# Performance work log

Hardware: AMD Instinct MI355X
Metric: run time of the kernel (lower is better)

## Reference

```python
import jax, jax.numpy as jnp
import numpy as np

IN_DIM = 512
ATT_DIM = 64
B, N = 4, 4096


def setup_inputs() -> dict:
    key = jax.random.key(0)
    k1, k2, k3, k4 = jax.random.split(key, 4)
    x = jax.random.normal(k1, (B, N, IN_DIM), dtype=jnp.float32)
    adj_matrix = (jax.random.uniform(k2, (B, N, N)) < 0.05).astype(jnp.float32)
    # nn.Linear weights: qk_nn (2*att_dim, in_dim), v_nn (in_dim, in_dim), no bias
    W_qk = jax.random.normal(k3, (2 * ATT_DIM, IN_DIM), dtype=jnp.float32) / np.sqrt(IN_DIM)
    W_v = jax.random.normal(k4, (IN_DIM, IN_DIM), dtype=jnp.float32) / np.sqrt(IN_DIM)
    return {"x": x, "adj_matrix": adj_matrix, "W_qk": W_qk, "W_v": W_v}


def reference(x, adj_matrix, W_qk, W_v):
    # q, k: (B, N, att_dim) from a single fused projection, then chunk
    qk = jnp.einsum('bnd,ed->bne', x, W_qk)
    q, k = jnp.split(qk, 2, axis=-1)
    v = jnp.einsum('bnd,ed->bne', x, W_v)  # (B, N, in_dim)
    inv_scale = 1.0 / (ATT_DIM ** 0.5)
    # dense NxN scores masked by adjacency, row-summed -> (B, N, 1)
    scores = jnp.einsum('bnd,bmd->bnm', q, k) * inv_scale
    w = jnp.sum(scores * adj_matrix, axis=-1, keepdims=True)
    w = jax.nn.softmax(w, axis=1)  # softmax over bag dimension N
    return w * v
```

## Files before the change

### kernel.cpp

```cpp
#include <hip/hip_runtime.h>
#include <hip/hip_bf16.h>

#define B_   4
#define N_   4096
#define IND  512
#define ATT  64
#define QKD  128

#define KSPLIT 4
#define KCHUNK 1024

typedef __attribute__((ext_vector_type(8))) short short8v;
typedef __attribute__((ext_vector_type(4))) float f32x4;

__device__ __forceinline__ void f8_to_bf16_hilo(const float4& v0, const float4& v1,
                                                short8v& hi, short8v& lo) {
  union { short8v v; unsigned short u[8]; } h, l;
  const float av[8] = {v0.x, v0.y, v0.z, v0.w, v1.x, v1.y, v1.z, v1.w};
#pragma unroll
  for (int j = 0; j < 8; ++j) {
    const unsigned short hu = (unsigned short)(__float_as_uint(av[j]) >> 16);
    const float fh = __uint_as_float((unsigned)hu << 16);
    h.u[j] = hu;
    l.u[j] = (unsigned short)(__float_as_uint(av[j] - fh) >> 16);
  }
  hi = h.v; lo = l.v;
}

__global__ __launch_bounds__(256)
void prep_frag(const float* __restrict__ src, unsigned short* __restrict__ dst,
               int nct) {
  const int wid = threadIdx.x >> 6, lane = threadIdx.x & 63;
  const int ct = blockIdx.x * 4 + wid;
  if (ct >= nct) return;
  const float* s = src + ((size_t)ct * 16 + (lane & 15)) * IND + ((lane >> 4) << 3);
  unsigned short* d = dst + (size_t)ct * 16 * 2 * 512 + (size_t)lane * 8;
#pragma unroll 4
  for (int slab = 0; slab < 16; ++slab) {
    const float4 v0 = *(const float4*)(s + slab * 32);
    const float4 v1 = *(const float4*)(s + slab * 32 + 4);
    short8v hv, lv;
    f8_to_bf16_hilo(v0, v1, hv, lv);
    *(short8v*)(d + (size_t)slab * 2 * 512)       = hv;
    *(short8v*)(d + (size_t)slab * 2 * 512 + 512) = lv;
  }
}

__global__ __launch_bounds__(256, 2)
void gemm_mfma(const unsigned short* __restrict__ xf,
               const unsigned short* __restrict__ wf,
               float* __restrict__ C, int Nout) {
  const int lane = threadIdx.x & 63;
  const int wid  = threadIdx.x >> 6;
  const int g0   = blockIdx.x * 64 + wid * 16;
  const int mt   = g0 >> 4;
  const int ct0  = blockIdx.y * 8;

  const unsigned short* xb = xf + (size_t)mt * 16 * 2 * 512 + (size_t)lane * 8;
  const unsigned short* wb = wf + (size_t)ct0 * 16 * 2 * 512 + (size_t)lane * 8;

  f32x4 acc[8] = {{0.f,0.f,0.f,0.f},{0.f,0.f,0.f,0.f},{0.f,0.f,0.f,0.f},
                  {0.f,0.f,0.f,0.f},{0.f,0.f,0.f,0.f},{0.f,0.f,0.f,0.f},
                  {0.f,0.f,0.f,0.f},{0.f,0.f,0.f,0.f}};

  short8v axh = *(const short8v*)(xb);
  short8v axl = *(const short8v*)(xb + 512);

  for (int slab = 0; slab < 16; ++slab) {
    const int sn = (slab < 15) ? slab + 1 : 15;
    const short8v nxh = *(const short8v*)(xb + (size_t)sn * 1024);
    const short8v nxl = *(const short8v*)(xb + (size_t)sn * 1024 + 512);

#pragma unroll
    for (int c = 0; c < 8; ++c) {
      const unsigned short* wp = wb + ((size_t)(c * 16 + slab) * 2) * 512;
      const short8v bh = *(const short8v*)(wp);
      const short8v bl = *(const short8v*)(wp + 512);
      acc[c] = __builtin_amdgcn_mfma_f32_16x16x32_bf16(axh, bh, acc[c], 0, 0, 0);
      acc[c] = __builtin_amdgcn_mfma_f32_16x16x32_bf16(axl, bh, acc[c], 0, 0, 0);
      acc[c] = __builtin_amdgcn_mfma_f32_16x16x32_bf16(axh, bl, acc[c], 0, 0, 0);
    }
    axh = nxh; axl = nxl;
  }

  float* outp = C + ((size_t)g0 + ((lane >> 4) << 2)) * Nout + ct0 * 16 + (lane & 15);
#pragma unroll
  for (int c = 0; c < 8; ++c)
#pragma unroll
    for (int r = 0; r < 4; ++r)
      outp[(size_t)r * Nout + c * 16] = acc[c][r];
}

__global__ __launch_bounds__(256)
void prep_k(const float* __restrict__ qk, unsigned short* __restrict__ ktf) {
  __shared__ unsigned short sh[32][68];
  __shared__ unsigned short sl[32][68];
  const int b    = blockIdx.x >> 7;
  const int slab = blockIdx.x & 127;
  const int t = threadIdx.x;

#pragma unroll
  for (int i = 0; i < 2; ++i) {
    const int f = t + i * 256;
    const int ml  = f >> 4;
    const int ch4 = (f & 15) << 2;
    const float4 v = *(const float4*)(qk +
        ((size_t)b * N_ + slab * 32 + ml) * QKD + ATT + ch4);
    const float vv[4] = {v.x, v.y, v.z, v.w};
#pragma unroll
    for (int j = 0; j < 4; ++j) {
      const unsigned short hi = (unsigned short)(__float_as_uint(vv[j]) >> 16);
      const float fhi = __uint_as_float((unsigned)hi << 16);
      const unsigned short lo = (unsigned short)(__float_as_uint(vv[j] - fhi) >> 16);
      sh[ml][ch4 + j] = hi;
      sl[ml][ch4 + j] = lo;
    }
  }
  __syncthreads();

  const int lane = t & 63;
  const int c    = t >> 6;
  const int mb   = (lane >> 4) << 3;
  const int ch   = c * 16 + (lane & 15);
  unsigned short* outb = ktf +
      (((size_t)(b * 128 + slab) * 4 + c) * 2) * 512 + (size_t)lane * 8;
  union { short8v v; unsigned short u[8]; } hv, lv;
#pragma unroll
  for (int j = 0; j < 8; ++j) {
    hv.u[j] = sh[mb + j][ch];
    lv.u[j] = sl[mb + j][ch];
  }
  *(short8v*)(outb)       = hv.v;
  *(short8v*)(outb + 512) = lv.v;
}

__global__ __launch_bounds__(256, 2)
void adjk_mfma(const float* __restrict__ adj,
               const unsigned short* __restrict__ ktf,
               float* __restrict__ kapart) {
  const int lane = threadIdx.x & 63;
  const int wid  = threadIdx.x >> 6;
  const int g0   = blockIdx.x * 128 + wid * 32;
  const int b    = g0 >> 12;
  const int split = blockIdx.y;
  const int k0   = split * KCHUNK;
  const int slab0 = k0 >> 5;

  const int arow = lane & 15;
  const int koff = (lane >> 4) << 3;

  const float* aptr0 = adj + (size_t)(g0 + arow) * N_ + k0 + koff;
  const float* aptr1 = aptr0 + (size_t)16 * N_;
  const unsigned short* kbase =
      ktf + (size_t)(b * 128 + slab0) * 4096 + (size_t)lane * 8;

  f32x4 acc[2][4] = {{{0.f,0.f,0.f,0.f},{0.f,0.f,0.f,0.f},
                      {0.f,0.f,0.f,0.f},{0.f,0.f,0.f,0.f}},
                     {{0.f,0.f,0.f,0.f},{0.f,0.f,0.f,0.f},
                      {0.f,0.f,0.f,0.f},{0.f,0.f,0.f,0.f}}};

  float4 a00 = *(const float4*)(aptr0);
  float4 a01 = *(const float4*)(aptr0 + 4);
  float4 a10 = *(const float4*)(aptr1);
  float4 a11 = *(const float4*)(aptr1 + 4);

  for (int s = 0; s < 32; ++s) {
    const unsigned short* kb = kbase + (size_t)s * 4096;
    const short8v b00 = *(const short8v*)(kb);
    const short8v b01 = *(const short8v*)(kb + 512);
    const short8v b10 = *(const short8v*)(kb + 1024);
    const short8v b11 = *(const short8v*)(kb + 1536);
    const short8v b20 = *(const short8v*)(kb + 2048);
    const short8v b21 = *(const short8v*)(kb + 2560);
    const short8v b30 = *(const short8v*)(kb + 3072);
    const short8v b31 = *(const short8v*)(kb + 3584);

    const int sn = (s < 31) ? s + 1 : 31;
    const float4 n00 = *(const float4*)(aptr0 + sn * 32);
    const float4 n01 = *(const float4*)(aptr0 + sn * 32 + 4);
    const float4 n10 = *(const float4*)(aptr1 + sn * 32);
    const float4 n11 = *(const float4*)(aptr1 + sn * 32 + 4);

    union { short8v v; unsigned short u[8]; } af0, af1;
    {
      const float av0[8] = {a00.x,a00.y,a00.z,a00.w,a01.x,a01.y,a01.z,a01.w};
      const float av1[8] = {a10.x,a10.y,a10.z,a10.w,a11.x,a11.y,a11.z,a11.w};
#pragma unroll
      for (int j = 0; j < 8; ++j) {
        af0.u[j] = (unsigned short)(__float_as_uint(av0[j]) >> 16);
        af1.u[j] = (unsigned short)(__float_as_uint(av1[j]) >> 16);
      }
    }

    acc[0][0] = __builtin_amdgcn_mfma_f32_16x16x32_bf16(af0.v, b00, acc[0][0], 0,0,0);
    acc[0][0] = __builtin_amdgcn_mfma_f32_16x16x32_bf16(af0.v, b01, acc[0][0], 0,0,0);
    acc[0][1] = __builtin_amdgcn_mfma_f32_16x16x32_bf16(af0.v, b10, acc[0][1], 0,0,0);
    acc[0][1] = __builtin_amdgcn_mfma_f32_16x16x32_bf16(af0.v, b11, acc[0][1], 0,0,0);
    acc[0][2] = __builtin_amdgcn_mfma_f32_16x16x32_bf16(af0.v, b20, acc[0][2], 0,0,0);
    acc[0][2] = __builtin_amdgcn_mfma_f32_16x16x32_bf16(af0.v, b21, acc[0][2], 0,0,0);
    acc[0][3] = __builtin_amdgcn_mfma_f32_16x16x32_bf16(af0.v, b30, acc[0][3], 0,0,0);
    acc[0][3] = __builtin_amdgcn_mfma_f32_16x16x32_bf16(af0.v, b31, acc[0][3], 0,0,0);
    acc[1][0] = __builtin_amdgcn_mfma_f32_16x16x32_bf16(af1.v, b00, acc[1][0], 0,0,0);
    acc[1][0] = __builtin_amdgcn_mfma_f32_16x16x32_bf16(af1.v, b01, acc[1][0], 0,0,0);
    acc[1][1] = __builtin_amdgcn_mfma_f32_16x16x32_bf16(af1.v, b10, acc[1][1], 0,0,0);
    acc[1][1] = __builtin_amdgcn_mfma_f32_16x16x32_bf16(af1.v, b11, acc[1][1], 0,0,0);
    acc[1][2] = __builtin_amdgcn_mfma_f32_16x16x32_bf16(af1.v, b20, acc[1][2], 0,0,0);
    acc[1][2] = __builtin_amdgcn_mfma_f32_16x16x32_bf16(af1.v, b21, acc[1][2], 0,0,0);
    acc[1][3] = __builtin_amdgcn_mfma_f32_16x16x32_bf16(af1.v, b30, acc[1][3], 0,0,0);
    acc[1][3] = __builtin_amdgcn_mfma_f32_16x16x32_bf16(af1.v, b31, acc[1][3], 0,0,0);

    a00 = n00; a01 = n01; a10 = n10; a11 = n11;
  }

#pragma unroll
  for (int tile = 0; tile < 2; ++tile) {
    float* outp = kapart +
        ((size_t)split * (B_ * N_) + g0 + tile * 16 + ((lane >> 4) << 2)) * ATT
        + (lane & 15);
#pragma unroll
    for (int c = 0; c < 4; ++c)
#pragma unroll
      for (int r = 0; r < 4; ++r)
        outp[(size_t)r * ATT + c * 16] = acc[tile][c][r];
  }
}

__global__ __launch_bounds__(256)
void qdot(const float* __restrict__ qk, const float* __restrict__ kapart,
          float* __restrict__ wpre) {
  const int wid  = threadIdx.x >> 6;
  const int lane = threadIdx.x & 63;
  const int row  = blockIdx.x * 4 + wid;

  float ka = 0.f;
#pragma unroll
  for (int s = 0; s < KSPLIT; ++s)
    ka += kapart[((size_t)s * B_ * N_ + row) * ATT + lane];

  const float q = qk[(size_t)row * QKD + lane];
  float val = q * ka;
#pragma unroll
  for (int off = 32; off; off >>= 1) val += __shfl_xor(val, off);
  if (lane == 0) wpre[row] = val * 0.125f;
}

__global__ __launch_bounds__(256)
void softmax_bag(float* __restrict__ w) {
  __shared__ float red[256];
  const int b = blockIdx.x;
  float* wb = w + (size_t)b * N_;
  const int t = threadIdx.x;

  float vals[16];
  float mx = -1e30f;
#pragma unroll
  for (int i = 0; i < 16; ++i) {
    vals[i] = wb[t + i * 256];
    mx = fmaxf(mx, vals[i]);
  }
  red[t] = mx; __syncthreads();
  for (int s = 128; s; s >>= 1) {
    if (t < s) red[t] = fmaxf(red[t], red[t + s]);
    __syncthreads();
  }
  mx = red[0];
  __syncthreads();

  float sum = 0.f;
#pragma unroll
  for (int i = 0; i < 16; ++i) {
    vals[i] = expf(vals[i] - mx);
    sum += vals[i];
  }
  red[t] = sum; __syncthreads();
  for (int s = 128; s; s >>= 1) {
    if (t < s) red[t] += red[t + s];
    __syncthreads();
  }
  const float inv = 1.f / red[0];
#pragma unroll
  for (int i = 0; i < 16; ++i) wb[t + i * 256] = vals[i] * inv;
}

__global__ __launch_bounds__(256)
void scale_v(float* __restrict__ out, const float* __restrict__ w, int total4) {
  int idx = blockIdx.x * blockDim.x + threadIdx.x;
  const int stride = gridDim.x * blockDim.x;
  for (; idx < total4; idx += stride) {
    float4 v = ((const float4*)out)[idx];
    const float s = w[idx >> 7];
    v.x *= s; v.y *= s; v.z *= s; v.w *= s;
    ((float4*)out)[idx] = v;
  }
}

extern "C" void kernel_launch(void* const* d_in, const int* in_sizes, int n_in,
                              void* d_out, int out_size, void* d_ws, size_t ws_size,
                              hipStream_t stream) {
  const float* x    = (const float*)d_in[0];
  const float* adj  = (const float*)d_in[1];
  const float* W_qk = (const float*)d_in[2];
  const float* W_v  = (const float*)d_in[3];
  float* out = (float*)d_out;

  float* qk     = (float*)d_ws;
  float* kapart = qk + (size_t)B_ * N_ * QKD;
  float* wpre   = kapart + (size_t)KSPLIT * B_ * N_ * ATT;
  unsigned short* ktf  = (unsigned short*)(wpre + B_ * N_);
  unsigned short* xft  = ktf + (size_t)B_ * 128 * 4096;
  unsigned short* wvf  = xft + (size_t)1024 * 16 * 2 * 512;
  unsigned short* wqkf = wvf + (size_t)32 * 16 * 2 * 512;

  const int M = B_ * N_;

  prep_frag<<<256, 256, 0, stream>>>(x, xft, 1024);
  prep_frag<<<8, 256, 0, stream>>>(W_v, wvf, 32);
  prep_frag<<<2, 256, 0, stream>>>(W_qk, wqkf, 8);

  {
    dim3 grid(M / 64, QKD / 128);
    gemm_mfma<<<grid, 256, 0, stream>>>(xft, wqkf, qk, QKD);
  }
  {
    dim3 grid(M / 64, IND / 128);
    gemm_mfma<<<grid, 256, 0, stream>>>(xft, wvf, out, IND);
  }
  prep_k<<<B_ * 128, 256, 0, stream>>>(qk, ktf);
  {
    dim3 grid(M / 128, KSPLIT);
    adjk_mfma<<<grid, 256, 0, stream>>>(adj, ktf, kapart);
  }
  qdot<<<M / 4, 256, 0, stream>>>(qk, kapart, wpre);
  softmax_bag<<<B_, 256, 0, stream>>>(wpre);
  const int total4 = M * (IND / 4);
  scale_v<<<2048, 256, 0, stream>>>(out, wpre, total4);
}
```

Measured before the change: 518.9 us.

## Stage adj/K tiles via async global-to-LDS loads and fuse softmax scaling into V GEMM

Replaces the register-prefetch adj×K kernel with an LDS double-buffered version that uses global_load_lds with an XOR swizzle to bring adjacency and K fragments into shared memory. KSPLIT drops from 4 to 2, so each block walks a longer K range and there are fewer partial sums. The V projection GEMM now runs after the softmax and multiplies by the weights in its epilogue, which removes the separate scale_v read-modify-write pass over the output. The 96KB shared-memory footprint limits occupancy to one block per CU and halves the grid of the dominant kernel.

```diff
diff --git a/kernel.cpp b/kernel.cpp
--- a/kernel.cpp
+++ b/kernel.cpp
@@ -7,11 +7,18 @@
 #define ATT  64
 #define QKD  128
 
-#define KSPLIT 4
-#define KCHUNK 1024
+#define KSPLIT 2
+#define KCHUNK 2048
+#define AK_NT  32
 
 typedef __attribute__((ext_vector_type(8))) short short8v;
 typedef __attribute__((ext_vector_type(4))) float f32x4;
+
+__device__ __forceinline__ void gload_lds16(const void* g, void* l) {
+  __builtin_amdgcn_global_load_lds(
+      (const __attribute__((address_space(1))) unsigned int*)g,
+      (__attribute__((address_space(3))) unsigned int*)l, 16, 0, 0);
+}
 
 __device__ __forceinline__ void f8_to_bf16_hilo(const float4& v0, const float4& v1,
                                                 short8v& hi, short8v& lo) {
@@ -49,7 +56,8 @@
 __global__ __launch_bounds__(256, 2)
 void gemm_mfma(const unsigned short* __restrict__ xf,
                const unsigned short* __restrict__ wf,
-               float* __restrict__ C, int Nout) {
+               float* __restrict__ C, int Nout,
+               const float* __restrict__ wsc) {
   const int lane = threadIdx.x & 63;
   const int wid  = threadIdx.x >> 6;
   const int g0   = blockIdx.x * 64 + wid * 16;
@@ -85,10 +93,12 @@
 
   float* outp = C + ((size_t)g0 + ((lane >> 4) << 2)) * Nout + ct0 * 16 + (lane & 15);
 #pragma unroll
-  for (int c = 0; c < 8; ++c)
-#pragma unroll
-    for (int r = 0; r < 4; ++r)
-      outp[(size_t)r * Nout + c * 16] = acc[c][r];
+  for (int r = 0; r < 4; ++r) {
+    const float s = wsc ? wsc[g0 + ((lane >> 4) << 2) + r] : 1.0f;
+#pragma unroll
+    for (int c = 0; c < 8; ++c)
+      outp[(size_t)r * Nout + c * 16] = acc[c][r] * s;
+  }
 }
 
 __global__ __launch_bounds__(256)
@@ -134,94 +144,106 @@
   *(short8v*)(outb + 512) = lv.v;
 }
 
-__global__ __launch_bounds__(256, 2)
-void adjk_mfma(const float* __restrict__ adj,
-               const unsigned short* __restrict__ ktf,
-               float* __restrict__ kapart) {
+__global__ __launch_bounds__(256)
+void adjk_lds(const float* __restrict__ adj,
+              const unsigned short* __restrict__ ktf,
+              float* __restrict__ kapart) {
+  __shared__ __align__(16) unsigned char smem[98304];
   const int lane = threadIdx.x & 63;
   const int wid  = threadIdx.x >> 6;
-  const int g0   = blockIdx.x * 128 + wid * 32;
+  const int g0   = blockIdx.x * 128;
   const int b    = g0 >> 12;
   const int split = blockIdx.y;
   const int k0   = split * KCHUNK;
-  const int slab0 = k0 >> 5;
-
-  const int arow = lane & 15;
-  const int koff = (lane >> 4) << 3;
-
-  const float* aptr0 = adj + (size_t)(g0 + arow) * N_ + k0 + koff;
-  const float* aptr1 = aptr0 + (size_t)16 * N_;
-  const unsigned short* kbase =
-      ktf + (size_t)(b * 128 + slab0) * 4096 + (size_t)lane * 8;
+
+  const int lr   = lane >> 4;
+  const int cch  = lane & 15;
+
+  auto STAGE = [&](int t, int buf) {
+    const int kt = k0 + t * 64;
+    {
+      const int rbase = wid * 32;
+#pragma unroll
+      for (int i = 0; i < 8; ++i) {
+        const int r = rbase + i * 4 + lr;
+        const int csrc = cch ^ (r & 7);
+        const float* src = adj + (size_t)(g0 + r) * N_ + kt + csrc * 4;
+        void* dst = smem + buf * 32768 + (rbase + i * 4) * 256;
+        gload_lds16(src, dst);
+      }
+    }
+    {
+      const unsigned short* kb = ktf + ((size_t)b * 128 + (kt >> 5)) * 4096;
+#pragma unroll
+      for (int j = 0; j < 4; ++j) {
+        const unsigned short* src = kb + (wid * 4 + j) * 512 + lane * 8;
+        void* dst = smem + 65536 + buf * 16384 + (wid * 4 + j) * 1024;
+        gload_lds16(src, dst);
+      }
+    }
+  };
 
   f32x4 acc[2][4] = {{{0.f,0.f,0.f,0.f},{0.f,0.f,0.f,0.f},
                       {0.f,0.f,0.f,0.f},{0.f,0.f,0.f,0.f}},
                      {{0.f,0.f,0.f,0.f},{0.f,0.f,0.f,0.f},
                       {0.f,0.f,0.f,0.f},{0.f,0.f,0.f,0.f}}};
 
-  float4 a00 = *(const float4*)(aptr0);
-  float4 a01 = *(const float4*)(aptr0 + 4);
-  float4 a10 = *(const float4*)(aptr1);
-  float4 a11 = *(const float4*)(aptr1 + 4);
-
-  for (int s = 0; s < 32; ++s) {
-    const unsigned short* kb = kbase + (size_t)s * 4096;
-    const short8v b00 = *(const short8v*)(kb);
-    const short8v b01 = *(const short8v*)(kb + 512);
-    const short8v b10 = *(const short8v*)(kb + 1024);
-    const short8v b11 = *(const short8v*)(kb + 1536);
-    const short8v b20 = *(const short8v*)(kb + 2048);
-    const short8v b21 = *(const short8v*)(kb + 2560);
-    const short8v b30 = *(const short8v*)(kb + 3072);
-    const short8v b31 = *(const short8v*)(kb + 3584);
-
-    const int sn = (s < 31) ? s + 1 : 31;
-    const float4 n00 = *(const float4*)(aptr0 + sn * 32);
-    const float4 n01 = *(const float4*)(aptr0 + sn * 32 + 4);
-    const float4 n10 = *(const float4*)(aptr1 + sn * 32);
-    const float4 n11 = *(const float4*)(aptr1 + sn * 32 + 4);
-
-    union { short8v v; unsigned short u[8]; } af0, af1;
-    {
-      const float av0[8] = {a00.x,a00.y,a00.z,a00.w,a01.x,a01.y,a01.z,a01.w};
-      const float av1[8] = {a10.x,a10.y,a10.z,a10.w,a11.x,a11.y,a11.z,a11.w};
-#pragma unroll
-      for (int j = 0; j < 8; ++j) {
-        af0.u[j] = (unsigned short)(__float_as_uint(av0[j]) >> 16);
-        af1.u[j] = (unsigned short)(__float_as_uint(av1[j]) >> 16);
+  STAGE(0, 0);
+  __syncthreads();
+
+  for (int t = 0; t < AK_NT; ++t) {
+    const int cur = t & 1;
+    if (t + 1 < AK_NT) STAGE(t + 1, cur ^ 1);
+
+    const float* A = (const float*)(smem + cur * 32768);
+    const unsigned short* Bp = (const unsigned short*)(smem + 65536 + cur * 16384);
+
+#pragma unroll
+    for (int s2 = 0; s2 < 2; ++s2) {
+      const unsigned short* bb = Bp + s2 * 4096 + lane * 8;
+      const short8v b0h = *(const short8v*)(bb);
+      const short8v b0l = *(const short8v*)(bb + 512);
+      const short8v b1h = *(const short8v*)(bb + 1024);
+      const short8v b1l = *(const short8v*)(bb + 1536);
+      const short8v b2h = *(const short8v*)(bb + 2048);
+      const short8v b2l = *(const short8v*)(bb + 2560);
+      const short8v b3h = *(const short8v*)(bb + 3072);
+      const short8v b3l = *(const short8v*)(bb + 3584);
+
+#pragma unroll
+      for (int rt = 0; rt < 2; ++rt) {
+        const int r = wid * 32 + rt * 16 + cch;
+        const int cb = s2 * 8 + (lr << 1);
+        const f32x4 a0 = *(const f32x4*)(A + r * 64 + ((cb ^ (r & 7)) << 2));
+        const f32x4 a1 = *(const f32x4*)(A + r * 64 + (((cb + 1) ^ (r & 7)) << 2));
+        union { short8v v; unsigned short u[8]; } af;
+#pragma unroll
+        for (int j = 0; j < 4; ++j) {
+          af.u[j]     = (unsigned short)(__float_as_uint(a0[j]) >> 16);
+          af.u[4 + j] = (unsigned short)(__float_as_uint(a1[j]) >> 16);
+        }
+        acc[rt][0] = __builtin_amdgcn_mfma_f32_16x16x32_bf16(af.v, b0h, acc[rt][0], 0,0,0);
+        acc[rt][0] = __builtin_amdgcn_mfma_f32_16x16x32_bf16(af.v, b0l, acc[rt][0], 0,0,0);
+        acc[rt][1] = __builtin_amdgcn_mfma_f32_16x16x32_bf16(af.v, b1h, acc[rt][1], 0,0,0);
+        acc[rt][1] = __builtin_amdgcn_mfma_f32_16x16x32_bf16(af.v, b1l, acc[rt][1], 0,0,0);
+        acc[rt][2] = __builtin_amdgcn_mfma_f32_16x16x32_bf16(af.v, b2h, acc[rt][2], 0,0,0);
+        acc[rt][2] = __builtin_amdgcn_mfma_f32_16x16x32_bf16(af.v, b2l, acc[rt][2], 0,0,0);
+        acc[rt][3] = __builtin_amdgcn_mfma_f32_16x16x32_bf16(af.v, b3h, acc[rt][3], 0,0,0);
+        acc[rt][3] = __builtin_amdgcn_mfma_f32_16x16x32_bf16(af.v, b3l, acc[rt][3], 0,0,0);
       }
     }
-
-    acc[0][0] = __builtin_amdgcn_mfma_f32_16x16x32_bf16(af0.v, b00, acc[0][0], 0,0,0);
-    acc[0][0] = __builtin_amdgcn_mfma_f32_16x16x32_bf16(af0.v, b01, acc[0][0], 0,0,0);
-    acc[0][1] = __builtin_amdgcn_mfma_f32_16x16x32_bf16(af0.v, b10, acc[0][1], 0,0,0);
-    acc[0][1] = __builtin_amdgcn_mfma_f32_16x16x32_bf16(af0.v, b11, acc[0][1], 0,0,0);
-    acc[0][2] = __builtin_amdgcn_mfma_f32_16x16x32_bf16(af0.v, b20, acc[0][2], 0,0,0);
-    acc[0][2] = __builtin_amdgcn_mfma_f32_16x16x32_bf16(af0.v, b21, acc[0][2], 0,0,0);
-    acc[0][3] = __builtin_amdgcn_mfma_f32_16x16x32_bf16(af0.v, b30, acc[0][3], 0,0,0);
-    acc[0][3] = __builtin_amdgcn_mfma_f32_16x16x32_bf16(af0.v, b31, acc[0][3], 0,0,0);
-    acc[1][0] = __builtin_amdgcn_mfma_f32_16x16x32_bf16(af1.v, b00, acc[1][0], 0,0,0);
-    acc[1][0] = __builtin_amdgcn_mfma_f32_16x16x32_bf16(af1.v, b01, acc[1][0], 0,0,0);
-    acc[1][1] = __builtin_amdgcn_mfma_f32_16x16x32_bf16(af1.v, b10, acc[1][1], 0,0,0);
-    acc[1][1] = __builtin_amdgcn_mfma_f32_16x16x32_bf16(af1.v, b11, acc[1][1], 0,0,0);
-    acc[1][2] = __builtin_amdgcn_mfma_f32_16x16x32_bf16(af1.v, b20, acc[1][2], 0,0,0);
-    acc[1][2] = __builtin_amdgcn_mfma_f32_16x16x32_bf16(af1.v, b21, acc[1][2], 0,0,0);
-    acc[1][3] = __builtin_amdgcn_mfma_f32_16x16x32_bf16(af1.v, b30, acc[1][3], 0,0,0);
-    acc[1][3] = __builtin_amdgcn_mfma_f32_16x16x32_bf16(af1.v, b31, acc[1][3], 0,0,0);
-
-    a00 = n00; a01 = n01; a10 = n10; a11 = n11;
-  }
-
-#pragma unroll
-  for (int tile = 0; tile < 2; ++tile) {
+    __syncthreads();
+  }
+
+#pragma unroll
+  for (int rt = 0; rt < 2; ++rt) {
     float* outp = kapart +
-        ((size_t)split * (B_ * N_) + g0 + tile * 16 + ((lane >> 4) << 2)) * ATT
-        + (lane & 15);
+        ((size_t)split * (B_ * N_) + g0 + wid * 32 + rt * 16 + (lr << 2)) * ATT + cch;
 #pragma unroll
     for (int c = 0; c < 4; ++c)
 #pragma unroll
       for (int r = 0; r < 4; ++r)
-        outp[(size_t)r * ATT + c * 16] = acc[tile][c][r];
+        outp[(size_t)r * ATT + c * 16] = acc[rt][c][r];
   }
 }
 
@@ -280,18 +302,6 @@
   const float inv = 1.f / red[0];
 #pragma unroll
   for (int i = 0; i < 16; ++i) wb[t + i * 256] = vals[i] * inv;
-}
-
-__global__ __launch_bounds__(256)
-void scale_v(float* __restrict__ out, const float* __restrict__ w, int total4) {
-  int idx = blockIdx.x * blockDim.x + threadIdx.x;
-  const int stride = gridDim.x * blockDim.x;
-  for (; idx < total4; idx += stride) {
-    float4 v = ((const float4*)out)[idx];
-    const float s = w[idx >> 7];
-    v.x *= s; v.y *= s; v.z *= s; v.w *= s;
-    ((float4*)out)[idx] = v;
-  }
 }
 
 extern "C" void kernel_launch(void* const* d_in, const int* in_sizes, int n_in,
@@ -319,19 +329,17 @@
 
   {
     dim3 grid(M / 64, QKD / 128);
-    gemm_mfma<<<grid, 256, 0, stream>>>(xft, wqkf, qk, QKD);
-  }
-  {
-    dim3 grid(M / 64, IND / 128);
-    gemm_mfma<<<grid, 256, 0, stream>>>(xft, wvf, out, IND);
+    gemm_mfma<<<grid, 256, 0, stream>>>(xft, wqkf, qk, QKD, nullptr);
   }
   prep_k<<<B_ * 128, 256, 0, stream>>>(qk, ktf);
   {
     dim3 grid(M / 128, KSPLIT);
-    adjk_mfma<<<grid, 256, 0, stream>>>(adj, ktf, kapart);
+    adjk_lds<<<grid, 256, 0, stream>>>(adj, ktf, kapart);
   }
   qdot<<<M / 4, 256, 0, stream>>>(qk, kapart, wpre);
   softmax_bag<<<B_, 256, 0, stream>>>(wpre);
-  const int total4 = M * (IND / 4);
-  scale_v<<<2048, 256, 0, stream>>>(out, wpre, total4);
-}
+  {
+    dim3 grid(M / 64, IND / 128);
+    gemm_mfma<<<grid, 256, 0, stream>>>(xft, wvf, out, IND, wpre);
+  }
+}
```

New measurement: 514.6 us. Within noise of the previous version (-0.8%).

## Bit-pack adjacency into a mask and fuse softmax scaling into the V GEMM

Applied to the files above, without the earlier changes.

Adds a streaming pass that compresses the fp32 adjacency into one bit per entry. The adj·K MFMA kernel then reads that 8 MB mask and expands the bits into bf16 ones and zeros, instead of loading and truncating fp32 tiles inside the MFMA loop. It also reorders the launches so the softmax weights exist before the V projection, which applies them as a per-row scale in its epilogue and removes the separate scale_v pass over the output. The mask only holds for binary adjacency values, and the full fp32 adjacency is still read once by the new packing kernel.

```diff
diff --git a/kernel.cpp b/kernel.cpp
--- a/kernel.cpp
+++ b/kernel.cpp
@@ -25,6 +25,27 @@
     l.u[j] = (unsigned short)(__float_as_uint(av[j] - fh) >> 16);
   }
   hi = h.v; lo = l.v;
+}
+
+__global__ __launch_bounds__(256)
+void pack_adj(const float* __restrict__ adj, unsigned char* __restrict__ mask) {
+  const size_t total = (size_t)B_ * N_ * (N_ / 8);
+  size_t i = (size_t)blockIdx.x * 256 + threadIdx.x;
+  const size_t stride = (size_t)gridDim.x * 256;
+  for (; i < total; i += stride) {
+    const float4 v0 = *(const float4*)(adj + i * 8);
+    const float4 v1 = *(const float4*)(adj + i * 8 + 4);
+    unsigned b = 0;
+    b |= (v0.x != 0.f) ? 1u   : 0u;
+    b |= (v0.y != 0.f) ? 2u   : 0u;
+    b |= (v0.z != 0.f) ? 4u   : 0u;
+    b |= (v0.w != 0.f) ? 8u   : 0u;
+    b |= (v1.x != 0.f) ? 16u  : 0u;
+    b |= (v1.y != 0.f) ? 32u  : 0u;
+    b |= (v1.z != 0.f) ? 64u  : 0u;
+    b |= (v1.w != 0.f) ? 128u : 0u;
+    mask[i] = (unsigned char)b;
+  }
 }
 
 __global__ __launch_bounds__(256)
@@ -49,7 +70,8 @@
 __global__ __launch_bounds__(256, 2)
 void gemm_mfma(const unsigned short* __restrict__ xf,
                const unsigned short* __restrict__ wf,
-               float* __restrict__ C, int Nout) {
+               float* __restrict__ C, int Nout,
+               const float* __restrict__ wsc) {
   const int lane = threadIdx.x & 63;
   const int wid  = threadIdx.x >> 6;
   const int g0   = blockIdx.x * 64 + wid * 16;
@@ -85,10 +107,12 @@
 
   float* outp = C + ((size_t)g0 + ((lane >> 4) << 2)) * Nout + ct0 * 16 + (lane & 15);
 #pragma unroll
-  for (int c = 0; c < 8; ++c)
-#pragma unroll
-    for (int r = 0; r < 4; ++r)
-      outp[(size_t)r * Nout + c * 16] = acc[c][r];
+  for (int r = 0; r < 4; ++r) {
+    const float s = wsc ? wsc[g0 + ((lane >> 4) << 2) + r] : 1.0f;
+#pragma unroll
+    for (int c = 0; c < 8; ++c)
+      outp[(size_t)r * Nout + c * 16] = acc[c][r] * s;
+  }
 }
 
 __global__ __launch_bounds__(256)
@@ -134,95 +158,65 @@
   *(short8v*)(outb + 512) = lv.v;
 }
 
-__global__ __launch_bounds__(256, 2)
-void adjk_mfma(const float* __restrict__ adj,
+__global__ __launch_bounds__(256, 4)
+void adjk_bits(const unsigned char* __restrict__ mask,
                const unsigned short* __restrict__ ktf,
                float* __restrict__ kapart) {
   const int lane = threadIdx.x & 63;
   const int wid  = threadIdx.x >> 6;
-  const int g0   = blockIdx.x * 128 + wid * 32;
+  const int g0   = blockIdx.x * 64 + wid * 16;
   const int b    = g0 >> 12;
   const int split = blockIdx.y;
-  const int k0   = split * KCHUNK;
-  const int slab0 = k0 >> 5;
-
-  const int arow = lane & 15;
-  const int koff = (lane >> 4) << 3;
-
-  const float* aptr0 = adj + (size_t)(g0 + arow) * N_ + k0 + koff;
-  const float* aptr1 = aptr0 + (size_t)16 * N_;
+  const int slab0 = split * 32;
+
+  const int lr  = lane >> 4;
+  const int cch = lane & 15;
+  const int bitoff = lr << 3;
+
+  const unsigned int* mrow =
+      (const unsigned int*)mask + (size_t)(g0 + cch) * (N_ / 32) + slab0;
   const unsigned short* kbase =
-      ktf + (size_t)(b * 128 + slab0) * 4096 + (size_t)lane * 8;
-
-  f32x4 acc[2][4] = {{{0.f,0.f,0.f,0.f},{0.f,0.f,0.f,0.f},
-                      {0.f,0.f,0.f,0.f},{0.f,0.f,0.f,0.f}},
-                     {{0.f,0.f,0.f,0.f},{0.f,0.f,0.f,0.f},
-                      {0.f,0.f,0.f,0.f},{0.f,0.f,0.f,0.f}}};
-
-  float4 a00 = *(const float4*)(aptr0);
-  float4 a01 = *(const float4*)(aptr0 + 4);
-  float4 a10 = *(const float4*)(aptr1);
-  float4 a11 = *(const float4*)(aptr1 + 4);
-
+      ktf + ((size_t)b * 128 + slab0) * 4096 + (size_t)lane * 8;
+
+  f32x4 acc[4] = {{0.f,0.f,0.f,0.f},{0.f,0.f,0.f,0.f},
+                  {0.f,0.f,0.f,0.f},{0.f,0.f,0.f,0.f}};
+
+#pragma unroll 4
   for (int s = 0; s < 32; ++s) {
+    const unsigned int word = mrow[s];
+    const unsigned int byte = (word >> bitoff) & 0xffu;
+    union { short8v v; unsigned short u[8]; } af;
+#pragma unroll
+    for (int j = 0; j < 8; ++j)
+      af.u[j] = ((byte >> j) & 1u) ? (unsigned short)0x3F80 : (unsigned short)0;
+
     const unsigned short* kb = kbase + (size_t)s * 4096;
-    const short8v b00 = *(const short8v*)(kb);
-    const short8v b01 = *(const short8v*)(kb + 512);
-    const short8v b10 = *(const short8v*)(kb + 1024);
-    const short8v b11 = *(const short8v*)(kb + 1536);
-    const short8v b20 = *(const short8v*)(kb + 2048);
-    const short8v b21 = *(const short8v*)(kb + 2560);
-    const short8v b30 = *(const short8v*)(kb + 3072);
-    const short8v b31 = *(const short8v*)(kb + 3584);
-
-    const int sn = (s < 31) ? s + 1 : 31;
-    const float4 n00 = *(const float4*)(aptr0 + sn * 32);
-    const float4 n01 = *(const float4*)(aptr0 + sn * 32 + 4);
-    const float4 n10 = *(const float4*)(aptr1 + sn * 32);
-    const float4 n11 = *(const float4*)(aptr1 + sn * 32 + 4);
-
-    union { short8v v; unsigned short u[8]; } af0, af1;
-    {
-      const float av0[8] = {a00.x,a00.y,a00.z,a00.w,a01.x,a01.y,a01.z,a01.w};
-      const float av1[8] = {a10.x,a10.y,a10.z,a10.w,a11.x,a11.y,a11.z,a11.w};
-#pragma unroll
-      for (int j = 0; j < 8; ++j) {
-        af0.u[j] = (unsigned short)(__float_as_uint(av0[j]) >> 16);
-        af1.u[j] = (unsigned short)(__float_as_uint(av1[j]) >> 16);
-      }
-    }
-
-    acc[0][0] = __builtin_amdgcn_mfma_f32_16x16x32_bf16(af0.v, b00, acc[0][0], 0,0,0);
-    acc[0][0] = __builtin_amdgcn_mfma_f32_16x16x32_bf16(af0.v, b01, acc[0][0], 0,0,0);
-    acc[0][1] = __builtin_amdgcn_mfma_f32_16x16x32_bf16(af0.v, b10, acc[0][1], 0,0,0);
-    acc[0][1] = __builtin_amdgcn_mfma_f32_16x16x32_bf16(af0.v, b11, acc[0][1], 0,0,0);
-    acc[0][2] = __builtin_amdgcn_mfma_f32_16x16x32_bf16(af0.v, b20, acc[0][2], 0,0,0);
-    acc[0][2] = __builtin_amdgcn_mfma_f32_16x16x32_bf16(af0.v, b21, acc[0][2], 0,0,0);
-    acc[0][3] = __builtin_amdgcn_mfma_f32_16x16x32_bf16(af0.v, b30, acc[0][3], 0,0,0);
-    acc[0][3] = __builtin_amdgcn_mfma_f32_16x16x32_bf16(af0.v, b31, acc[0][3], 0,0,0);
-    acc[1][0] = __builtin_amdgcn_mfma_f32_16x16x32_bf16(af1.v, b00, acc[1][0], 0,0,0);
-    acc[1][0] = __builtin_amdgcn_mfma_f32_16x16x32_bf16(af1.v, b01, acc[1][0], 0,0,0);
-    acc[1][1] = __builtin_amdgcn_mfma_f32_16x16x32_bf16(af1.v, b10, acc[1][1], 0,0,0);
-    acc[1][1] = __builtin_amdgcn_mfma_f32_16x16x32_bf16(af1.v, b11, acc[1][1], 0,0,0);
-    acc[1][2] = __builtin_amdgcn_mfma_f32_16x16x32_bf16(af1.v, b20, acc[1][2], 0,0,0);
-    acc[1][2] = __builtin_amdgcn_mfma_f32_16x16x32_bf16(af1.v, b21, acc[1][2], 0,0,0);
-    acc[1][3] = __builtin_amdgcn_mfma_f32_16x16x32_bf16(af1.v, b30, acc[1][3], 0,0,0);
-    acc[1][3] = __builtin_amdgcn_mfma_f32_16x16x32_bf16(af1.v, b31, acc[1][3], 0,0,0);
-
-    a00 = n00; a01 = n01; a10 = n10; a11 = n11;
-  }
-
-#pragma unroll
-  for (int tile = 0; tile < 2; ++tile) {
-    float* outp = kapart +
-        ((size_t)split * (B_ * N_) + g0 + tile * 16 + ((lane >> 4) << 2)) * ATT
-        + (lane & 15);
-#pragma unroll
-    for (int c = 0; c < 4; ++c)
-#pragma unroll
-      for (int r = 0; r < 4; ++r)
-        outp[(size_t)r * ATT + c * 16] = acc[tile][c][r];
-  }
+    const short8v b0h = *(const short8v*)(kb);
+    const short8v b0l = *(const short8v*)(kb + 512);
+    const short8v b1h = *(const short8v*)(kb + 1024);
+    const short8v b1l = *(const short8v*)(kb + 1536);
+    const short8v b2h = *(const short8v*)(kb + 2048);
+    const short8v b2l = *(const short8v*)(kb + 2560);
+    const short8v b3h = *(const short8v*)(kb + 3072);
+    const short8v b3l = *(const short8v*)(kb + 3584);
+
+    acc[0] = __builtin_amdgcn_mfma_f32_16x16x32_bf16(af.v, b0h, acc[0], 0, 0, 0);
+    acc[0] = __builtin_amdgcn_mfma_f32_16x16x32_bf16(af.v, b0l, acc[0], 0, 0, 0);
+    acc[1] = __builtin_amdgcn_mfma_f32_16x16x32_bf16(af.v, b1h, acc[1], 0, 0, 0);
+    acc[1] = __builtin_amdgcn_mfma_f32_16x16x32_bf16(af.v, b1l, acc[1], 0, 0, 0);
+    acc[2] = __builtin_amdgcn_mfma_f32_16x16x32_bf16(af.v, b2h, acc[2], 0, 0, 0);
+    acc[2] = __builtin_amdgcn_mfma_f32_16x16x32_bf16(af.v, b2l, acc[2], 0, 0, 0);
+    acc[3] = __builtin_amdgcn_mfma_f32_16x16x32_bf16(af.v, b3h, acc[3], 0, 0, 0);
+    acc[3] = __builtin_amdgcn_mfma_f32_16x16x32_bf16(af.v, b3l, acc[3], 0, 0, 0);
+  }
+
+  float* outp = kapart +
+      ((size_t)split * (B_ * N_) + g0 + (lr << 2)) * ATT + cch;
+#pragma unroll
+  for (int c = 0; c < 4; ++c)
+#pragma unroll
+    for (int r = 0; r < 4; ++r)
+      outp[(size_t)r * ATT + c * 16] = acc[c][r];
 }
 
 __global__ __launch_bounds__(256)
@@ -280,18 +274,6 @@
   const float inv = 1.f / red[0];
 #pragma unroll
   for (int i = 0; i < 16; ++i) wb[t + i * 256] = vals[i] * inv;
-}
-
-__global__ __launch_bounds__(256)
-void scale_v(float* __restrict__ out, const float* __restrict__ w, int total4) {
-  int idx = blockIdx.x * blockDim.x + threadIdx.x;
-  const int stride = gridDim.x * blockDim.x;
-  for (; idx < total4; idx += stride) {
-    float4 v = ((const float4*)out)[idx];
-    const float s = w[idx >> 7];
-    v.x *= s; v.y *= s; v.z *= s; v.w *= s;
-    ((float4*)out)[idx] = v;
-  }
 }
 
 extern "C" void kernel_launch(void* const* d_in, const int* in_sizes, int n_in,
@@ -310,8 +292,11 @@
   unsigned short* xft  = ktf + (size_t)B_ * 128 * 4096;
   unsigned short* wvf  = xft + (size_t)1024 * 16 * 2 * 512;
   unsigned short* wqkf = wvf + (size_t)32 * 16 * 2 * 512;
+  unsigned char* mask  = (unsigned char*)(wqkf + (size_t)8 * 16 * 2 * 512);
 
   const int M = B_ * N_;
+
+  pack_adj<<<2048, 256, 0, stream>>>(adj, mask);
 
   prep_frag<<<256, 256, 0, stream>>>(x, xft, 1024);
   prep_frag<<<8, 256, 0, stream>>>(W_v, wvf, 32);
@@ -319,19 +304,17 @@
 
   {
     dim3 grid(M / 64, QKD / 128);
-    gemm_mfma<<<grid, 256, 0, stream>>>(xft, wqkf, qk, QKD);
-  }
+    gemm_mfma<<<grid, 256, 0, stream>>>(xft, wqkf, qk, QKD, nullptr);
+  }
+  prep_k<<<B_ * 128, 256, 0, stream>>>(qk, ktf);
+  {
+    dim3 grid(M / 64, KSPLIT);
+    adjk_bits<<<grid, 256, 0, stream>>>(mask, ktf, kapart);
+  }
+  qdot<<<M / 4, 256, 0, stream>>>(qk, kapart, wpre);
+  softmax_bag<<<B_, 256, 0, stream>>>(wpre);
   {
     dim3 grid(M / 64, IND / 128);
-    gemm_mfma<<<grid, 256, 0, stream>>>(xft, wvf, out, IND);
-  }
-  prep_k<<<B_ * 128, 256, 0, stream>>>(qk, ktf);
-  {
-    dim3 grid(M / 128, KSPLIT);
-    adjk_mfma<<<grid, 256, 0, stream>>>(adj, ktf, kapart);
-  }
-  qdot<<<M / 4, 256, 0, stream>>>(qk, kapart, wpre);
-  softmax_bag<<<B_, 256, 0, stream>>>(wpre);
-  const int total4 = M * (IND / 4);
-  scale_v<<<2048, 256, 0, stream>>>(out, wpre, total4);
-}
+    gemm_mfma<<<grid, 256, 0, stream>>>(xft, wvf, out, IND, wpre);
+  }
+}
```

After: 535.3 us. 1.03x slower.
